# Kernel optimization log

Measured on AMD Instinct MI355X. Metric: run time of the kernel, lower is better.

## Reference

```python
import jax, jax.numpy as jnp
import numpy as np

D, H, L, N, BINS, V = 256, 8, 4, 512, 64, 20
DFF = 4 * D
DH = D // H
LAMBDA_RG = 10.0
STEPS = 10


def _lin(x, W, b):
    # torch nn.Linear convention: W is [out, in]
    return jnp.einsum('...i,oi->...o', x, W) + b


def _ln(x, g, b, eps=1e-5):
    m = x.mean(-1, keepdims=True)
    v = ((x - m) ** 2).mean(-1, keepdims=True)
    return (x - m) / jnp.sqrt(v + eps) * g + b


def _gelu(x):
    return jax.nn.gelu(x, approximate=False)  # torch nn.GELU default = exact erf


def _pos_encoding():
    pos = jnp.arange(N, dtype=jnp.float32)[:, None]
    div = jnp.exp(jnp.arange(0, D, 2, dtype=jnp.float32) * (-np.log(10000.0) / D))
    pe = jnp.zeros((N, D), jnp.float32)
    pe = pe.at[:, 0::2].set(jnp.sin(pos * div))
    pe = pe.at[:, 1::2].set(jnp.cos(pos * div))
    return pe


def _encoder_layer(x, Wqkv, bqkv, Wo, bo, g1, b1n, W1, b1, W2, b2, g2, b2n):
    # post-norm TransformerEncoderLayer, relu FFN, dropout=0 (eval)
    B, n, _ = x.shape
    qkv = _lin(x, Wqkv, bqkv)
    q, k, v = jnp.split(qkv, 3, axis=-1)
    hd = lambda t: t.reshape(B, n, H, DH).transpose(0, 2, 1, 3)
    q, k, v = hd(q), hd(k), hd(v)
    scores = jnp.einsum('bhqd,bhkd->bhqk', q, k) / jnp.sqrt(jnp.float32(DH))
    attn = jax.nn.softmax(scores, axis=-1)
    o = jnp.einsum('bhqk,bhkd->bhqd', attn, v).transpose(0, 2, 1, 3).reshape(B, n, D)
    x = _ln(x + _lin(o, Wo, bo), g1, b1n)
    ff = _lin(jax.nn.relu(_lin(x, W1, b1)), W2, b2)
    return _ln(x + ff, g2, b2n)


def setup_inputs() -> dict:
    key = jax.random.key(0)
    ks = list(jax.random.split(key, 24))
    it = iter(ks)
    w = lambda shape: jax.random.normal(next(it), shape, jnp.float32) * 0.02
    inp = {
        'tokens': jax.random.randint(next(it), (1, N), 0, V, dtype=jnp.int32),
        'noise': jax.random.normal(next(it), (1, N, 3), jnp.float32),
        'emb': w((V, D)),
        'Wqkv': w((L, 3 * D, D)), 'bqkv': jnp.zeros((L, 3 * D), jnp.float32),
        'Wo': w((L, D, D)), 'bo': jnp.zeros((L, D), jnp.float32),
        'ln1_g': jnp.ones((L, D), jnp.float32), 'ln1_b': jnp.zeros((L, D), jnp.float32),
        'W1': w((L, DFF, D)), 'b1': jnp.zeros((L, DFF), jnp.float32),
        'W2': w((L, D, DFF)), 'b2': jnp.zeros((L, D), jnp.float32),
        'ln2_g': jnp.ones((L, D), jnp.float32), 'ln2_b': jnp.zeros((L, D), jnp.float32),
        'aW1': w((D, D)), 'ab1': jnp.zeros((D,), jnp.float32),
        'aW2': w((1, D)), 'ab2': jnp.zeros((1,), jnp.float32),
        'cW': w((D, D)), 'cb': jnp.zeros((D,), jnp.float32),
        'dW1': w((D, 2 * D)), 'db1': jnp.zeros((D,), jnp.float32),
        'dW2': w((BINS, D)), 'db2': jnp.zeros((BINS,), jnp.float32),
        'tW1': w((D, D)), 'tb1': jnp.zeros((D,), jnp.float32),
        'tW2': w((2, D)), 'tb2': jnp.zeros((2,), jnp.float32),
        'pW': w((3, D)), 'pb': jnp.zeros((3,), jnp.float32),
    }
    return inp


def _forward(tokens, noise, emb, Wqkv, bqkv, Wo, bo, ln1_g, ln1_b, W1, b1, W2, b2,
             ln2_g, ln2_b, aW1, ab1, aW2, ab2, cW, cb, dW1, db1, dW2, db2,
             tW1, tb1, tW2, tb2, pW, pb):
    x = emb[tokens] + _pos_encoding()[None]  # [1,N,D]
    for l in range(L):
        x = _encoder_layer(x, Wqkv[l], bqkv[l], Wo[l], bo[l], ln1_g[l], ln1_b[l],
                           W1[l], b1[l], W2[l], b2[l], ln2_g[l], ln2_b[l])
    # AdaptiveAlphaPredictor
    a = jax.nn.sigmoid(_lin(_gelu(_lin(x, aW1, ab1)), aW2, ab2))
    alpha = (1.2 + a * (3.5 - 1.2))[..., 0]  # [1,N]
    # CSOCKernelAttention: distance power-law * exp-decay kernel
    idx = jnp.arange(N, dtype=jnp.float32)
    r = jnp.abs(idx[:, None] - idx[None, :]) + 1e-4  # [N,N]
    alpha_pair = (alpha[..., :, None] + alpha[..., None, :]) * 0.5  # [1,N,N]
    kernel = r[None] ** (-alpha_pair) * jnp.exp(-r[None] / LAMBDA_RG)
    kernel = kernel / (kernel.sum(-1, keepdims=True) + 1e-8)
    latent = jnp.einsum('bij,bjd->bid', kernel, x)
    # ContactPriorHead
    h = _lin(latent, cW, cb)
    contact = jax.nn.sigmoid(jnp.einsum('bid,bjd->bij', h, h))
    # DistogramHead: expand+concat+MLP (memory-bound O(N^2 d))
    xi = jnp.broadcast_to(latent[:, :, None, :], (1, N, N, D))
    xj = jnp.broadcast_to(latent[:, None, :, :], (1, N, N, D))
    pair = jnp.concatenate([xi, xj], axis=-1)  # [1,N,N,2D]
    disto = _lin(_gelu(_lin(pair, dW1, db1)), dW2, db2)  # [1,N,N,BINS]
    # TorsionGenerator
    t = _lin(_gelu(_lin(latent, tW1, tb1)), tW2, tb2)
    phi = jnp.tanh(t[..., 0]) * np.pi
    psi = jnp.tanh(t[..., 1]) * np.pi
    # DiffusionCoordinateInitializer (STEPS is a small fixed constant)
    target = _lin(latent, pW, pb)  # [1,N,3]
    c = noise
    for step in reversed(range(STEPS)):
        a_t = (step + 1) / STEPS
        c = a_t * c + (1.0 - a_t) * target
    return latent, alpha, contact, disto, phi, psi, c


def reference(tokens, noise, emb, Wqkv, bqkv, Wo, bo, ln1_g, ln1_b, W1, b1, W2, b2,
              ln2_g, ln2_b, aW1, ab1, aW2, ab2, cW, cb, dW1, db1, dW2, db2,
              tW1, tb1, tW2, tb2, pW, pb):
    return _forward(tokens, noise, emb, Wqkv, bqkv, Wo, bo, ln1_g, ln1_b, W1, b1,
                    W2, b2, ln2_g, ln2_b, aW1, ab1, aW2, ab2, cW, cb, dW1, db1,
                    dW2, db2, tW1, tb1, tW2, tb2, pW, pb)
```

## Files before the change

### kernel.cpp

```cpp
#include <hip/hip_runtime.h>
#include <hip/hip_bf16.h>

typedef __attribute__((ext_vector_type(8))) short bf16x8;
typedef __attribute__((ext_vector_type(4))) float f32x4;
typedef unsigned short ushort;

#define OFF_QKV 0
#define OFF_WO  786432
#define OFF_W1  1048576
#define OFF_W2  2097152
#define OFF_AW1 3145728
#define OFF_CW  3211264
#define OFF_DW1 3276800
#define OFF_TW1 3407872
#define WB_TOTAL 3473408

__device__ inline float gelu_f(float x) {
    return 0.5f * x * (1.0f + erff(x * 0.70710678118654752f));
}

__device__ inline ushort f2bfu(float x) {
    __hip_bfloat16 b = __float2bfloat16(x);
    return *reinterpret_cast<ushort*>(&b);
}

__device__ inline uint4 pack_bf8(float4 a, float4 b) {
    uint4 p;
    p.x = f2bfu(a.x) | ((unsigned)f2bfu(a.y) << 16);
    p.y = f2bfu(a.z) | ((unsigned)f2bfu(a.w) << 16);
    p.z = f2bfu(b.x) | ((unsigned)f2bfu(b.y) << 16);
    p.w = f2bfu(b.z) | ((unsigned)f2bfu(b.w) << 16);
    return p;
}

__device__ inline float wave_sum(float v) {
#pragma unroll
    for (int o = 32; o > 0; o >>= 1) v += __shfl_xor(v, o);
    return v;
}
__device__ inline float wave_max(float v) {
#pragma unroll
    for (int o = 32; o > 0; o >>= 1) v = fmaxf(v, __shfl_xor(v, o));
    return v;
}

__global__ void convw_k(const float* __restrict__ Wqkv, const float* __restrict__ Wo,
                        const float* __restrict__ W1, const float* __restrict__ W2,
                        const float* __restrict__ aW1, const float* __restrict__ cW,
                        const float* __restrict__ dW1, const float* __restrict__ tW1,
                        ushort* __restrict__ dst) {
    size_t i = ((size_t)blockIdx.x * 256 + threadIdx.x) * 8;
    if (i >= WB_TOTAL) return;
    const float* src;
    size_t off;
    if (i < OFF_WO)        { src = Wqkv; off = i; }
    else if (i < OFF_W1)   { src = Wo;   off = i - OFF_WO; }
    else if (i < OFF_W2)   { src = W1;   off = i - OFF_W1; }
    else if (i < OFF_AW1)  { src = W2;   off = i - OFF_W2; }
    else if (i < OFF_CW)   { src = aW1;  off = i - OFF_AW1; }
    else if (i < OFF_DW1)  { src = cW;   off = i - OFF_CW; }
    else if (i < OFF_TW1)  { src = dW1;  off = i - OFF_DW1; }
    else                   { src = tW1;  off = i - OFF_TW1; }
    float4 f0 = *(const float4*)&src[off];
    float4 f1 = *(const float4*)&src[off + 4];
    *(uint4*)&dst[i] = pack_bf8(f0, f1);
}

__global__ void embed_k(const int* __restrict__ tokens, const float* __restrict__ emb,
                        float* __restrict__ x, ushort* __restrict__ xb) {
    int n = blockIdx.x, t = threadIdx.x;
    float e = emb[(size_t)tokens[n] * 256 + t];
    int k = t >> 1;
    float div = expf((float)(2 * k) * (-9.210340371976184f / 256.0f));
    float arg = (float)n * div;
    float v = e + ((t & 1) ? cosf(arg) : sinf(arg));
    x[(size_t)n * 256 + t] = v;
    xb[(size_t)n * 256 + t] = f2bfu(v);
}

template <int ACT, int OBF>
__global__ __launch_bounds__(256) void gemm_bf(const ushort* __restrict__ A,
                                               const ushort* __restrict__ Wb,
                                               const float* __restrict__ bias,
                                               float* __restrict__ C,
                                               ushort* __restrict__ Cb,
                                               int Nn, int K, int lda, int ldw, int koff,
                                               size_t woff, size_t boff) {
    __shared__ ushort Al[2][2048];
    __shared__ ushort Wl[2][2048];
    const int t = threadIdx.x;
    const int bm = blockIdx.y * 64, bn = blockIdx.x * 64;
    const int lane = t & 63, wv = t >> 6;
    const int lo = lane & 15, hi = lane >> 4;

    const ushort* aptr = A + (size_t)(bm + lane) * lda + wv * 8;
    const ushort* wptr = Wb + woff + (size_t)(bn + lane) * ldw + koff + wv * 8;

    f32x4 acc0 = {0.f, 0.f, 0.f, 0.f}, acc1 = acc0, acc2 = acc0, acc3 = acc0;
    uint4 a = *(const uint4*)aptr;
    uint4 w = *(const uint4*)wptr;
    const int nsteps = K >> 5;
    for (int s = 0; s < nsteps; ++s) {
        const int buf = s & 1;
        *(uint4*)&Al[buf][t * 8] = a;
        *(uint4*)&Wl[buf][t * 8] = w;
        __syncthreads();
        if (s + 1 < nsteps) {
            a = *(const uint4*)(aptr + (s + 1) * 32);
            w = *(const uint4*)(wptr + (s + 1) * 32);
        }
        bf16x8 af = *(bf16x8*)&Al[buf][(hi * 64 + wv * 16 + lo) * 8];
        bf16x8 b0 = *(bf16x8*)&Wl[buf][(hi * 64 + 0 + lo) * 8];
        bf16x8 b1 = *(bf16x8*)&Wl[buf][(hi * 64 + 16 + lo) * 8];
        bf16x8 b2 = *(bf16x8*)&Wl[buf][(hi * 64 + 32 + lo) * 8];
        bf16x8 b3 = *(bf16x8*)&Wl[buf][(hi * 64 + 48 + lo) * 8];
        acc0 = __builtin_amdgcn_mfma_f32_16x16x32_bf16(af, b0, acc0, 0, 0, 0);
        acc1 = __builtin_amdgcn_mfma_f32_16x16x32_bf16(af, b1, acc1, 0, 0, 0);
        acc2 = __builtin_amdgcn_mfma_f32_16x16x32_bf16(af, b2, acc2, 0, 0, 0);
        acc3 = __builtin_amdgcn_mfma_f32_16x16x32_bf16(af, b3, acc3, 0, 0, 0);
    }

    float bv0 = bias ? bias[boff + bn + 0 + lo] : 0.0f;
    float bv1 = bias ? bias[boff + bn + 16 + lo] : 0.0f;
    float bv2 = bias ? bias[boff + bn + 32 + lo] : 0.0f;
    float bv3 = bias ? bias[boff + bn + 48 + lo] : 0.0f;
#pragma unroll
    for (int r = 0; r < 4; ++r) {
        size_t rw = (size_t)(bm + wv * 16 + hi * 4 + r) * Nn + bn;
        float v0 = acc0[r] + bv0, v1 = acc1[r] + bv1, v2 = acc2[r] + bv2, v3 = acc3[r] + bv3;
        if (ACT == 1) {
            v0 = fmaxf(v0, 0.f); v1 = fmaxf(v1, 0.f); v2 = fmaxf(v2, 0.f); v3 = fmaxf(v3, 0.f);
        }
        if (ACT == 2) {
            v0 = gelu_f(v0); v1 = gelu_f(v1); v2 = gelu_f(v2); v3 = gelu_f(v3);
        }
        if (OBF) {
            Cb[rw + 0 + lo] = f2bfu(v0);
            Cb[rw + 16 + lo] = f2bfu(v1);
            Cb[rw + 32 + lo] = f2bfu(v2);
            Cb[rw + 48 + lo] = f2bfu(v3);
        } else {
            C[rw + 0 + lo] = v0;
            C[rw + 16 + lo] = v1;
            C[rw + 32 + lo] = v2;
            C[rw + 48 + lo] = v3;
        }
    }
}

__global__ __launch_bounds__(256) void attn_k(const float* __restrict__ qkv,
                                              ushort* __restrict__ ob) {
    __shared__ float sc[4][512];
    int t = threadIdx.x;
    int w = t >> 6, lane = t & 63;
    int q = blockIdx.x * 4 + w;
    int h = blockIdx.y;
    const float* qptr = qkv + (size_t)q * 768 + h * 32;
    const float* kbase = qkv + 256 + h * 32;
    const float* vbase = qkv + 512 + h * 32;
    float qv[32];
#pragma unroll
    for (int d = 0; d < 32; d += 4) {
        float4 f = *(const float4*)(qptr + d);
        qv[d] = f.x; qv[d + 1] = f.y; qv[d + 2] = f.z; qv[d + 3] = f.w;
    }
    float mx = -1e30f;
    for (int k = lane; k < 512; k += 64) {
        const float* kp = kbase + (size_t)k * 768;
        float s = 0.0f;
#pragma unroll
        for (int d = 0; d < 32; d += 4) {
            float4 f = *(const float4*)(kp + d);
            s = fmaf(qv[d], f.x, s); s = fmaf(qv[d + 1], f.y, s);
            s = fmaf(qv[d + 2], f.z, s); s = fmaf(qv[d + 3], f.w, s);
        }
        s *= 0.17677669529663687f;
        sc[w][k] = s;
        mx = fmaxf(mx, s);
    }
    mx = wave_max(mx);
    float sum = 0.0f;
    for (int k = lane; k < 512; k += 64) {
        float e = expf(sc[w][k] - mx);
        sc[w][k] = e;
        sum += e;
    }
    sum = wave_sum(sum);
    float inv = 1.0f / sum;
    __syncthreads();
    int d = lane & 31, half = lane >> 5;
    const float* vp = vbase + d;
    const int kb = half * 256;
    float a0 = 0.f, a1 = 0.f, a2 = 0.f, a3 = 0.f;
    float a4 = 0.f, a5 = 0.f, a6 = 0.f, a7 = 0.f;
    for (int k = kb; k < kb + 256; k += 8) {
        float4 p0 = *(const float4*)&sc[w][k];
        float4 p1 = *(const float4*)&sc[w][k + 4];
        a0 = fmaf(p0.x, vp[(size_t)(k + 0) * 768], a0);
        a1 = fmaf(p0.y, vp[(size_t)(k + 1) * 768], a1);
        a2 = fmaf(p0.z, vp[(size_t)(k + 2) * 768], a2);
        a3 = fmaf(p0.w, vp[(size_t)(k + 3) * 768], a3);
        a4 = fmaf(p1.x, vp[(size_t)(k + 4) * 768], a4);
        a5 = fmaf(p1.y, vp[(size_t)(k + 5) * 768], a5);
        a6 = fmaf(p1.z, vp[(size_t)(k + 6) * 768], a6);
        a7 = fmaf(p1.w, vp[(size_t)(k + 7) * 768], a7);
    }
    float accv = ((a0 + a1) + (a2 + a3)) + ((a4 + a5) + (a6 + a7));
    accv += __shfl_down(accv, 32);
    if (lane < 32) ob[(size_t)q * 256 + h * 32 + d] = f2bfu(accv * inv);
}

__global__ void ln_res_k(float* __restrict__ x, const float* __restrict__ y,
                         const float* __restrict__ g, const float* __restrict__ b,
                         size_t goff, ushort* __restrict__ xb) {
    int row = blockIdx.x, t = threadIdx.x;
    __shared__ float red[8];
    float v = x[row * 256 + t] + y[row * 256 + t];
    float s = wave_sum(v);
    if ((t & 63) == 0) red[t >> 6] = s;
    __syncthreads();
    float mean = (red[0] + red[1] + red[2] + red[3]) * (1.0f / 256.0f);
    float d = v - mean;
    float s2 = wave_sum(d * d);
    if ((t & 63) == 0) red[4 + (t >> 6)] = s2;
    __syncthreads();
    float var = (red[4] + red[5] + red[6] + red[7]) * (1.0f / 256.0f);
    float res = d * rsqrtf(var + 1e-5f) * g[goff + t] + b[goff + t];
    x[row * 256 + t] = res;
    xb[row * 256 + t] = f2bfu(res);
}

__global__ void alpha_k(const float* __restrict__ t1, const float* __restrict__ aW2,
                        const float* __restrict__ ab2, float* __restrict__ alphaf,
                        float* __restrict__ out_alpha) {
    int t = threadIdx.x, w = t >> 6, lane = t & 63;
    int n = blockIdx.x * 4 + w;
    const float* r = t1 + (size_t)n * 256;
    float s = 0.0f;
    for (int d = lane; d < 256; d += 64) s = fmaf(r[d], aW2[d], s);
    s = wave_sum(s);
    if (lane == 0) {
        float z = s + ab2[0];
        float a = 1.0f / (1.0f + expf(-z));
        float al = 1.2f + 2.3f * a;
        alphaf[n] = al;
        out_alpha[n] = al;
    }
}

__global__ void csock_k(const float* __restrict__ x, const float* __restrict__ alphaf,
                        float* __restrict__ latent, float* __restrict__ out_latent,
                        ushort* __restrict__ latentb) {
    int i = blockIdx.x, t = threadIdx.x;
    __shared__ float wgt[512];
    __shared__ float red[4];
    float ai = alphaf[i];
    float lsum = 0.0f;
    for (int j = t; j < 512; j += 256) {
        float r = fabsf((float)(i - j)) + 1e-4f;
        float ap = 0.5f * (ai + alphaf[j]);
        float wv = powf(r, -ap) * expf(-r * 0.1f);
        wgt[j] = wv;
        lsum += wv;
    }
    float s = wave_sum(lsum);
    if ((t & 63) == 0) red[t >> 6] = s;
    __syncthreads();
    float S = red[0] + red[1] + red[2] + red[3] + 1e-8f;
    float acc = 0.0f;
    for (int j = 0; j < 512; ++j) acc = fmaf(wgt[j], x[(size_t)j * 256 + t], acc);
    float res = acc / S;
    latent[(size_t)i * 256 + t] = res;
    out_latent[(size_t)i * 256 + t] = res;
    latentb[(size_t)i * 256 + t] = f2bfu(res);
}

__global__ void contact_k(const float* __restrict__ h, float* __restrict__ out) {
    int i = blockIdx.x, t = threadIdx.x;
    __shared__ float hi[256];
    hi[t] = h[(size_t)i * 256 + t];
    __syncthreads();
    for (int j = t; j < 512; j += 256) {
        const float* hj = h + (size_t)j * 256;
        float s = 0.0f;
#pragma unroll 4
        for (int d = 0; d < 256; d += 4) {
            float4 a = *(const float4*)&hi[d];
            float4 b = *(const float4*)&hj[d];
            s = fmaf(a.x, b.x, s); s = fmaf(a.y, b.y, s);
            s = fmaf(a.z, b.z, s); s = fmaf(a.w, b.w, s);
        }
        out[(size_t)i * 512 + j] = 1.0f / (1.0f + expf(-s));
    }
}

__global__ __launch_bounds__(256) void disto_k(const float* __restrict__ U,
                                               const float* __restrict__ V,
                                               const float* __restrict__ dW2,
                                               const float* __restrict__ db2,
                                               float* __restrict__ out) {
    __shared__ short hsl[32 * 64 * 8];
    __shared__ short w2l[32 * 64 * 8];
    const int t = threadIdx.x;
    const int i = blockIdx.x;
    const int row = t >> 2;
    const int dq = t & 3;

#pragma unroll
    for (int c = 0; c < 8; ++c) {
        int dblk = dq * 8 + c;
        int d0 = dblk * 8;
        float4 w0 = *(const float4*)&dW2[(size_t)row * 256 + d0];
        float4 w1 = *(const float4*)&dW2[(size_t)row * 256 + d0 + 4];
        *(uint4*)&w2l[(dblk * 64 + row) * 8] = pack_bf8(w0, w1);
    }

    const int wv = t >> 6, lane = t & 63;
    const int lo = lane & 15, hi = lane >> 4;
    const int jw = wv * 16;
    float dbv[4];
#pragma unroll
    for (int nt = 0; nt < 4; ++nt) dbv[nt] = db2[nt * 16 + lo];

    for (int p = 0; p < 8; ++p) {
        const int j0 = p * 64;
#pragma unroll
        for (int c = 0; c < 8; ++c) {
            int dblk = dq * 8 + c;
            int d0 = dblk * 8;
            float4 u0 = *(const float4*)&U[(size_t)i * 256 + d0];
            float4 u1 = *(const float4*)&U[(size_t)i * 256 + d0 + 4];
            float4 v0 = *(const float4*)&V[(size_t)(j0 + row) * 256 + d0];
            float4 v1 = *(const float4*)&V[(size_t)(j0 + row) * 256 + d0 + 4];
            float4 h0, h1;
            h0.x = gelu_f(u0.x + v0.x); h0.y = gelu_f(u0.y + v0.y);
            h0.z = gelu_f(u0.z + v0.z); h0.w = gelu_f(u0.w + v0.w);
            h1.x = gelu_f(u1.x + v1.x); h1.y = gelu_f(u1.y + v1.y);
            h1.z = gelu_f(u1.z + v1.z); h1.w = gelu_f(u1.w + v1.w);
            *(uint4*)&hsl[(dblk * 64 + row) * 8] = pack_bf8(h0, h1);
        }
        __syncthreads();

        f32x4 acc0 = {0.f, 0.f, 0.f, 0.f}, acc1 = acc0, acc2 = acc0, acc3 = acc0;
#pragma unroll
        for (int kk = 0; kk < 8; ++kk) {
            int db = kk * 4 + hi;
            bf16x8 a = *(bf16x8*)&hsl[(db * 64 + jw + lo) * 8];
            bf16x8 b0 = *(bf16x8*)&w2l[(db * 64 + 0 + lo) * 8];
            bf16x8 b1 = *(bf16x8*)&w2l[(db * 64 + 16 + lo) * 8];
            bf16x8 b2 = *(bf16x8*)&w2l[(db * 64 + 32 + lo) * 8];
            bf16x8 b3 = *(bf16x8*)&w2l[(db * 64 + 48 + lo) * 8];
            acc0 = __builtin_amdgcn_mfma_f32_16x16x32_bf16(a, b0, acc0, 0, 0, 0);
            acc1 = __builtin_amdgcn_mfma_f32_16x16x32_bf16(a, b1, acc1, 0, 0, 0);
            acc2 = __builtin_amdgcn_mfma_f32_16x16x32_bf16(a, b2, acc2, 0, 0, 0);
            acc3 = __builtin_amdgcn_mfma_f32_16x16x32_bf16(a, b3, acc3, 0, 0, 0);
        }
#pragma unroll
        for (int r = 0; r < 4; ++r) {
            size_t jg = (size_t)i * 512 + j0 + jw + hi * 4 + r;
            out[jg * 64 + 0 + lo] = acc0[r] + dbv[0];
            out[jg * 64 + 16 + lo] = acc1[r] + dbv[1];
            out[jg * 64 + 32 + lo] = acc2[r] + dbv[2];
            out[jg * 64 + 48 + lo] = acc3[r] + dbv[3];
        }
        __syncthreads();
    }
}

__global__ void torsion_k(const float* __restrict__ t1, const float* __restrict__ tW2,
                          const float* __restrict__ tb2, float* __restrict__ phi,
                          float* __restrict__ psi) {
    int t = threadIdx.x, w = t >> 6, lane = t & 63;
    int n = blockIdx.x * 4 + w;
    const float* r = t1 + (size_t)n * 256;
    float s0 = 0.0f, s1 = 0.0f;
    for (int d = lane; d < 256; d += 64) {
        float v = r[d];
        s0 = fmaf(v, tW2[d], s0);
        s1 = fmaf(v, tW2[256 + d], s1);
    }
    s0 = wave_sum(s0);
    s1 = wave_sum(s1);
    if (lane == 0) {
        phi[n] = tanhf(s0 + tb2[0]) * 3.14159265358979323846f;
        psi[n] = tanhf(s1 + tb2[1]) * 3.14159265358979323846f;
    }
}

__global__ void diff_k(const float* __restrict__ latent, const float* __restrict__ pW,
                       const float* __restrict__ pb, const float* __restrict__ noise,
                       float* __restrict__ outc) {
    int idx = blockIdx.x * 256 + threadIdx.x;
    if (idx >= 512 * 3) return;
    int n = idx / 3, a = idx % 3;
    const float* r = latent + (size_t)n * 256;
    float s = pb[a];
    for (int d = 0; d < 256; ++d) s = fmaf(r[d], pW[(size_t)a * 256 + d], s);
    float c = noise[idx];
#pragma unroll
    for (int st = 9; st >= 0; --st) {
        float at = (float)(st + 1) * 0.1f;
        c = at * c + (1.0f - at) * s;
    }
    outc[idx] = c;
}

extern "C" void kernel_launch(void* const* d_in, const int* in_sizes, int n_in,
                              void* d_out, int out_size, void* d_ws, size_t ws_size,
                              hipStream_t stream) {
    const int* tokens  = (const int*)d_in[0];
    const float* noise = (const float*)d_in[1];
    const float* emb   = (const float*)d_in[2];
    const float* Wqkv  = (const float*)d_in[3];
    const float* bqkv  = (const float*)d_in[4];
    const float* Wo    = (const float*)d_in[5];
    const float* bo    = (const float*)d_in[6];
    const float* ln1_g = (const float*)d_in[7];
    const float* ln1_b = (const float*)d_in[8];
    const float* W1    = (const float*)d_in[9];
    const float* b1    = (const float*)d_in[10];
    const float* W2    = (const float*)d_in[11];
    const float* b2    = (const float*)d_in[12];
    const float* ln2_g = (const float*)d_in[13];
    const float* ln2_b = (const float*)d_in[14];
    const float* aW1   = (const float*)d_in[15];
    const float* ab1   = (const float*)d_in[16];
    const float* aW2   = (const float*)d_in[17];
    const float* ab2   = (const float*)d_in[18];
    const float* cW    = (const float*)d_in[19];
    const float* cb    = (const float*)d_in[20];
    const float* dW1   = (const float*)d_in[21];
    const float* db1   = (const float*)d_in[22];
    const float* dW2   = (const float*)d_in[23];
    const float* db2   = (const float*)d_in[24];
    const float* tW1   = (const float*)d_in[25];
    const float* tb1   = (const float*)d_in[26];
    const float* tW2   = (const float*)d_in[27];
    const float* tb2   = (const float*)d_in[28];
    const float* pW    = (const float*)d_in[29];
    const float* pb    = (const float*)d_in[30];

    float* out         = (float*)d_out;
    float* out_latent  = out;
    float* out_alpha   = out + 131072;
    float* out_contact = out + 131584;
    float* out_disto   = out + 393728;
    float* out_phi     = out + 17170944;
    float* out_psi     = out + 17171456;
    float* out_c       = out + 17171968;

    float* scratch = out_disto;
    float* x    = scratch;
    float* qkv  = scratch + 131072;
    float* y    = scratch + 1179648;
    float* hbuf = scratch + 1310720;
    float* t1   = scratch + 1441792;
    ushort* wb      = (ushort*)(scratch + 2000000);
    ushort* xb      = (ushort*)(scratch + 3740000);
    ushort* ob      = (ushort*)(scratch + 3810000);
    ushort* ffhb    = (ushort*)(scratch + 3880000);
    ushort* latentb = (ushort*)(scratch + 4150000);

    float* latentf = (float*)d_ws;
    float* U       = latentf + 131072;
    float* Vv      = U + 131072;
    float* alphaf  = Vv + 131072;

    convw_k<<<1696, 256, 0, stream>>>(Wqkv, Wo, W1, W2, aW1, cW, dW1, tW1, wb);
    embed_k<<<512, 256, 0, stream>>>(tokens, emb, x, xb);

    for (int l = 0; l < 4; ++l) {
        gemm_bf<0, 0><<<dim3(12, 8), 256, 0, stream>>>(xb, wb, bqkv, qkv, nullptr,
                                                       768, 256, 256, 256, 0,
                                                       OFF_QKV + (size_t)l * 196608, (size_t)l * 768);
        attn_k<<<dim3(128, 8), 256, 0, stream>>>(qkv, ob);
        gemm_bf<0, 0><<<dim3(4, 8), 256, 0, stream>>>(ob, wb, bo, y, nullptr,
                                                      256, 256, 256, 256, 0,
                                                      OFF_WO + (size_t)l * 65536, (size_t)l * 256);
        ln_res_k<<<512, 256, 0, stream>>>(x, y, ln1_g, ln1_b, (size_t)l * 256, xb);
        gemm_bf<1, 1><<<dim3(16, 8), 256, 0, stream>>>(xb, wb, b1, nullptr, ffhb,
                                                       1024, 256, 256, 256, 0,
                                                       OFF_W1 + (size_t)l * 262144, (size_t)l * 1024);
        gemm_bf<0, 0><<<dim3(4, 8), 256, 0, stream>>>(ffhb, wb, b2, y, nullptr,
                                                      256, 1024, 1024, 1024, 0,
                                                      OFF_W2 + (size_t)l * 262144, (size_t)l * 256);
        ln_res_k<<<512, 256, 0, stream>>>(x, y, ln2_g, ln2_b, (size_t)l * 256, xb);
    }

    gemm_bf<2, 0><<<dim3(4, 8), 256, 0, stream>>>(xb, wb, ab1, t1, nullptr,
                                                  256, 256, 256, 256, 0, OFF_AW1, 0);
    alpha_k<<<128, 256, 0, stream>>>(t1, aW2, ab2, alphaf, out_alpha);

    csock_k<<<512, 256, 0, stream>>>(x, alphaf, latentf, out_latent, latentb);

    gemm_bf<0, 0><<<dim3(4, 8), 256, 0, stream>>>(latentb, wb, cb, hbuf, nullptr,
                                                  256, 256, 256, 256, 0, OFF_CW, 0);
    contact_k<<<512, 256, 0, stream>>>(hbuf, out_contact);

    gemm_bf<0, 0><<<dim3(4, 8), 256, 0, stream>>>(latentb, wb, db1, U, nullptr,
                                                  256, 256, 256, 512, 0, OFF_DW1, 0);
    gemm_bf<0, 0><<<dim3(4, 8), 256, 0, stream>>>(latentb, wb, nullptr, Vv, nullptr,
                                                  256, 256, 256, 512, 256, OFF_DW1, 0);

    gemm_bf<2, 0><<<dim3(4, 8), 256, 0, stream>>>(latentb, wb, tb1, t1, nullptr,
                                                  256, 256, 256, 256, 0, OFF_TW1, 0);
    torsion_k<<<128, 256, 0, stream>>>(t1, tW2, tb2, out_phi, out_psi);

    diff_k<<<6, 256, 0, stream>>>(latentf, pW, pb, noise, out_c);

    disto_k<<<512, 256, 0, stream>>>(U, Vv, dW2, db2, out_disto);
}
```

Measured before the change: 509.1 us.

## Fuse O-projection and FFN with residual LayerNorm; batch head GEMMs into one launch

```diff
diff --git a/kernel.cpp b/kernel.cpp
--- a/kernel.cpp
+++ b/kernel.cpp
@@ -148,6 +148,283 @@
     }
 }
 
+__global__ __launch_bounds__(256) void oproj_ln_k(const ushort* __restrict__ ob,
+                                                  const ushort* __restrict__ wbp,
+                                                  const float* __restrict__ bo,
+                                                  const float* __restrict__ g,
+                                                  const float* __restrict__ bln,
+                                                  float* __restrict__ x,
+                                                  ushort* __restrict__ xb,
+                                                  size_t woff, size_t boff, size_t goff) {
+    __shared__ ushort Al[2][2048];
+    __shared__ ushort Wl[2][8192];
+    const int t = threadIdx.x;
+    const int bm = blockIdx.x * 64;
+    const int lane = t & 63, wv = t >> 6;
+    const int lo = lane & 15, hi = lane >> 4;
+    const int arow = t >> 2, akg = t & 3;
+
+    const ushort* aptr = ob + (size_t)(bm + arow) * 256 + akg * 8;
+    const ushort* wptr = wbp + woff + akg * 8;
+
+    f32x4 acc[16];
+#pragma unroll
+    for (int i = 0; i < 16; ++i) acc[i] = (f32x4){0.f, 0.f, 0.f, 0.f};
+
+    uint4 apre = *(const uint4*)aptr;
+    uint4 wpre[4];
+#pragma unroll
+    for (int q = 0; q < 4; ++q)
+        wpre[q] = *(const uint4*)(wptr + (size_t)(q * 64 + arow) * 256);
+
+    for (int s = 0; s < 8; ++s) {
+        const int buf = s & 1;
+        *(uint4*)&Al[buf][(akg * 64 + arow) * 8] = apre;
+#pragma unroll
+        for (int q = 0; q < 4; ++q)
+            *(uint4*)&Wl[buf][(akg * 256 + q * 64 + arow) * 8] = wpre[q];
+        __syncthreads();
+        if (s < 7) {
+            apre = *(const uint4*)(aptr + (s + 1) * 32);
+#pragma unroll
+            for (int q = 0; q < 4; ++q)
+                wpre[q] = *(const uint4*)(wptr + (size_t)(q * 64 + arow) * 256 + (s + 1) * 32);
+        }
+        bf16x8 af = *(bf16x8*)&Al[buf][(hi * 64 + wv * 16 + lo) * 8];
+#pragma unroll
+        for (int nt = 0; nt < 16; ++nt) {
+            bf16x8 bf = *(bf16x8*)&Wl[buf][(hi * 256 + nt * 16 + lo) * 8];
+            acc[nt] = __builtin_amdgcn_mfma_f32_16x16x32_bf16(af, bf, acc[nt], 0, 0, 0);
+        }
+    }
+
+    float bv[16], gg[16], bb[16];
+#pragma unroll
+    for (int nt = 0; nt < 16; ++nt) {
+        bv[nt] = bo[boff + nt * 16 + lo];
+        gg[nt] = g[goff + nt * 16 + lo];
+        bb[nt] = bln[goff + nt * 16 + lo];
+    }
+#pragma unroll
+    for (int r = 0; r < 4; ++r) {
+        int row = bm + wv * 16 + hi * 4 + r;
+        float part = 0.f;
+#pragma unroll
+        for (int nt = 0; nt < 16; ++nt) {
+            float xo = x[(size_t)row * 256 + nt * 16 + lo];
+            float v = acc[nt][r] + bv[nt] + xo;
+            acc[nt][r] = v;
+            part += v;
+        }
+        part += __shfl_xor(part, 1); part += __shfl_xor(part, 2);
+        part += __shfl_xor(part, 4); part += __shfl_xor(part, 8);
+        float mean = part * (1.0f / 256.0f);
+        float p2 = 0.f;
+#pragma unroll
+        for (int nt = 0; nt < 16; ++nt) { float d = acc[nt][r] - mean; p2 = fmaf(d, d, p2); }
+        p2 += __shfl_xor(p2, 1); p2 += __shfl_xor(p2, 2);
+        p2 += __shfl_xor(p2, 4); p2 += __shfl_xor(p2, 8);
+        float inv = rsqrtf(p2 * (1.0f / 256.0f) + 1e-5f);
+#pragma unroll
+        for (int nt = 0; nt < 16; ++nt) {
+            float res = (acc[nt][r] - mean) * inv * gg[nt] + bb[nt];
+            x[(size_t)row * 256 + nt * 16 + lo] = res;
+            xb[(size_t)row * 256 + nt * 16 + lo] = f2bfu(res);
+        }
+    }
+}
+
+__global__ __launch_bounds__(256) void ffn_ln_k(const ushort* __restrict__ xbin,
+                                                const ushort* __restrict__ wbp,
+                                                const float* __restrict__ b1,
+                                                const float* __restrict__ b2,
+                                                const float* __restrict__ g,
+                                                const float* __restrict__ bln,
+                                                float* __restrict__ x,
+                                                ushort* __restrict__ xb,
+                                                size_t w1off, size_t w2off,
+                                                size_t b1off, size_t b2off, size_t goff) {
+    __shared__ ushort Hl[32768];
+    __shared__ ushort Al[2][2048];
+    __shared__ ushort W1l[2][2048];
+    __shared__ ushort W2l[2][8192];
+    const int t = threadIdx.x;
+    const int bm = blockIdx.x * 64;
+    const int lane = t & 63, wv = t >> 6;
+    const int lo = lane & 15, hi = lane >> 4;
+    const int arow = t >> 2, akg = t & 3;
+    const ushort* aptr = xbin + (size_t)(bm + arow) * 256 + akg * 8;
+
+    f32x4 yacc[16];
+#pragma unroll
+    for (int i = 0; i < 16; ++i) yacc[i] = (f32x4){0.f, 0.f, 0.f, 0.f};
+
+    for (int half = 0; half < 2; ++half) {
+        for (int p = 0; p < 8; ++p) {
+            const int colbase = half * 512 + p * 64;
+            const ushort* w1ptr = wbp + w1off + (size_t)(colbase + arow) * 256 + akg * 8;
+            f32x4 pacc[4];
+#pragma unroll
+            for (int i = 0; i < 4; ++i) pacc[i] = (f32x4){0.f, 0.f, 0.f, 0.f};
+            uint4 apre = *(const uint4*)aptr;
+            uint4 w1pre = *(const uint4*)w1ptr;
+            for (int s = 0; s < 8; ++s) {
+                const int buf = s & 1;
+                *(uint4*)&Al[buf][(akg * 64 + arow) * 8] = apre;
+                *(uint4*)&W1l[buf][(akg * 64 + arow) * 8] = w1pre;
+                __syncthreads();
+                if (s < 7) {
+                    apre = *(const uint4*)(aptr + (s + 1) * 32);
+                    w1pre = *(const uint4*)(w1ptr + (s + 1) * 32);
+                }
+                bf16x8 af = *(bf16x8*)&Al[buf][(hi * 64 + wv * 16 + lo) * 8];
+#pragma unroll
+                for (int nt = 0; nt < 4; ++nt) {
+                    bf16x8 bf = *(bf16x8*)&W1l[buf][(hi * 64 + nt * 16 + lo) * 8];
+                    pacc[nt] = __builtin_amdgcn_mfma_f32_16x16x32_bf16(af, bf, pacc[nt], 0, 0, 0);
+                }
+            }
+#pragma unroll
+            for (int nt = 0; nt < 4; ++nt) {
+                float bvv = b1[b1off + colbase + nt * 16 + lo];
+#pragma unroll
+                for (int r = 0; r < 4; ++r) {
+                    float v = fmaxf(pacc[nt][r] + bvv, 0.f);
+                    int row = wv * 16 + hi * 4 + r;
+                    int cl = p * 64 + nt * 16 + lo;
+                    Hl[((cl >> 3) * 64 + row) * 8 + (cl & 7)] = f2bfu(v);
+                }
+            }
+        }
+        __syncthreads();
+
+        const ushort* w2ptr = wbp + w2off + (size_t)half * 512 + akg * 8;
+        uint4 w2pre[4];
+#pragma unroll
+        for (int q = 0; q < 4; ++q)
+            w2pre[q] = *(const uint4*)(w2ptr + (size_t)(q * 64 + arow) * 1024);
+        for (int s = 0; s < 16; ++s) {
+            const int buf = s & 1;
+#pragma unroll
+            for (int q = 0; q < 4; ++q)
+                *(uint4*)&W2l[buf][(akg * 256 + q * 64 + arow) * 8] = w2pre[q];
+            __syncthreads();
+            if (s < 15) {
+#pragma unroll
+                for (int q = 0; q < 4; ++q)
+                    w2pre[q] = *(const uint4*)(w2ptr + (size_t)(q * 64 + arow) * 1024 + (s + 1) * 32);
+            }
+            bf16x8 af = *(bf16x8*)&Hl[((s * 4 + hi) * 64 + wv * 16 + lo) * 8];
+#pragma unroll
+            for (int nt = 0; nt < 16; ++nt) {
+                bf16x8 bf = *(bf16x8*)&W2l[buf][(hi * 256 + nt * 16 + lo) * 8];
+                yacc[nt] = __builtin_amdgcn_mfma_f32_16x16x32_bf16(af, bf, yacc[nt], 0, 0, 0);
+            }
+        }
+        __syncthreads();
+    }
+
+    float bv[16], gg[16], bb[16];
+#pragma unroll
+    for (int nt = 0; nt < 16; ++nt) {
+        bv[nt] = b2[b2off + nt * 16 + lo];
+        gg[nt] = g[goff + nt * 16 + lo];
+        bb[nt] = bln[goff + nt * 16 + lo];
+    }
+#pragma unroll
+    for (int r = 0; r < 4; ++r) {
+        int row = bm + wv * 16 + hi * 4 + r;
+        float part = 0.f;
+#pragma unroll
+        for (int nt = 0; nt < 16; ++nt) {
+            float xo = x[(size_t)row * 256 + nt * 16 + lo];
+            float v = yacc[nt][r] + bv[nt] + xo;
+            yacc[nt][r] = v;
+            part += v;
+        }
+        part += __shfl_xor(part, 1); part += __shfl_xor(part, 2);
+        part += __shfl_xor(part, 4); part += __shfl_xor(part, 8);
+        float mean = part * (1.0f / 256.0f);
+        float p2 = 0.f;
+#pragma unroll
+        for (int nt = 0; nt < 16; ++nt) { float d = yacc[nt][r] - mean; p2 = fmaf(d, d, p2); }
+        p2 += __shfl_xor(p2, 1); p2 += __shfl_xor(p2, 2);
+        p2 += __shfl_xor(p2, 4); p2 += __shfl_xor(p2, 8);
+        float inv = rsqrtf(p2 * (1.0f / 256.0f) + 1e-5f);
+#pragma unroll
+        for (int nt = 0; nt < 16; ++nt) {
+            float res = (yacc[nt][r] - mean) * inv * gg[nt] + bb[nt];
+            x[(size_t)row * 256 + nt * 16 + lo] = res;
+            xb[(size_t)row * 256 + nt * 16 + lo] = f2bfu(res);
+        }
+    }
+}
+
+__global__ __launch_bounds__(256) void heads_k(const ushort* __restrict__ A,
+                                               const ushort* __restrict__ Wb,
+                                               const float* __restrict__ cb,
+                                               const float* __restrict__ db1,
+                                               const float* __restrict__ tb1,
+                                               float* __restrict__ hbuf,
+                                               float* __restrict__ U,
+                                               float* __restrict__ Vv,
+                                               float* __restrict__ t1t) {
+    size_t woff; int ldw, koff, act; const float* bias; float* C;
+    const int z = blockIdx.z;
+    if (z == 0)      { woff = OFF_CW;  ldw = 256; koff = 0;   bias = cb;      act = 0; C = hbuf; }
+    else if (z == 1) { woff = OFF_DW1; ldw = 512; koff = 0;   bias = db1;     act = 0; C = U; }
+    else if (z == 2) { woff = OFF_DW1; ldw = 512; koff = 256; bias = nullptr; act = 0; C = Vv; }
+    else             { woff = OFF_TW1; ldw = 256; koff = 0;   bias = tb1;     act = 2; C = t1t; }
+
+    __shared__ ushort Al[2][2048];
+    __shared__ ushort Wl[2][2048];
+    const int t = threadIdx.x;
+    const int bm = blockIdx.y * 64, bn = blockIdx.x * 64;
+    const int lane = t & 63, wv = t >> 6;
+    const int lo = lane & 15, hi = lane >> 4;
+
+    const ushort* aptr = A + (size_t)(bm + lane) * 256 + wv * 8;
+    const ushort* wptr = Wb + woff + (size_t)(bn + lane) * ldw + koff + wv * 8;
+
+    f32x4 acc0 = {0.f, 0.f, 0.f, 0.f}, acc1 = acc0, acc2 = acc0, acc3 = acc0;
+    uint4 a = *(const uint4*)aptr;
+    uint4 w = *(const uint4*)wptr;
+    for (int s = 0; s < 8; ++s) {
+        const int buf = s & 1;
+        *(uint4*)&Al[buf][t * 8] = a;
+        *(uint4*)&Wl[buf][t * 8] = w;
+        __syncthreads();
+        if (s < 7) {
+            a = *(const uint4*)(aptr + (s + 1) * 32);
+            w = *(const uint4*)(wptr + (s + 1) * 32);
+        }
+        bf16x8 af = *(bf16x8*)&Al[buf][(hi * 64 + wv * 16 + lo) * 8];
+        bf16x8 b0 = *(bf16x8*)&Wl[buf][(hi * 64 + 0 + lo) * 8];
+        bf16x8 b1 = *(bf16x8*)&Wl[buf][(hi * 64 + 16 + lo) * 8];
+        bf16x8 b2 = *(bf16x8*)&Wl[buf][(hi * 64 + 32 + lo) * 8];
+        bf16x8 b3 = *(bf16x8*)&Wl[buf][(hi * 64 + 48 + lo) * 8];
+        acc0 = __builtin_amdgcn_mfma_f32_16x16x32_bf16(af, b0, acc0, 0, 0, 0);
+        acc1 = __builtin_amdgcn_mfma_f32_16x16x32_bf16(af, b1, acc1, 0, 0, 0);
+        acc2 = __builtin_amdgcn_mfma_f32_16x16x32_bf16(af, b2, acc2, 0, 0, 0);
+        acc3 = __builtin_amdgcn_mfma_f32_16x16x32_bf16(af, b3, acc3, 0, 0, 0);
+    }
+
+    float bv0 = bias ? bias[bn + 0 + lo] : 0.0f;
+    float bv1 = bias ? bias[bn + 16 + lo] : 0.0f;
+    float bv2 = bias ? bias[bn + 32 + lo] : 0.0f;
+    float bv3 = bias ? bias[bn + 48 + lo] : 0.0f;
+#pragma unroll
+    for (int r = 0; r < 4; ++r) {
+        size_t rw = (size_t)(bm + wv * 16 + hi * 4 + r) * 256 + bn;
+        float v0 = acc0[r] + bv0, v1 = acc1[r] + bv1, v2 = acc2[r] + bv2, v3 = acc3[r] + bv3;
+        if (act == 2) { v0 = gelu_f(v0); v1 = gelu_f(v1); v2 = gelu_f(v2); v3 = gelu_f(v3); }
+        C[rw + 0 + lo] = v0;
+        C[rw + 16 + lo] = v1;
+        C[rw + 32 + lo] = v2;
+        C[rw + 48 + lo] = v3;
+    }
+}
+
 __global__ __launch_bounds__(256) void attn_k(const float* __restrict__ qkv,
                                               ushort* __restrict__ ob) {
     __shared__ float sc[4][512];
@@ -208,26 +485,6 @@
     float accv = ((a0 + a1) + (a2 + a3)) + ((a4 + a5) + (a6 + a7));
     accv += __shfl_down(accv, 32);
     if (lane < 32) ob[(size_t)q * 256 + h * 32 + d] = f2bfu(accv * inv);
-}
-
-__global__ void ln_res_k(float* __restrict__ x, const float* __restrict__ y,
-                         const float* __restrict__ g, const float* __restrict__ b,
-                         size_t goff, ushort* __restrict__ xb) {
-    int row = blockIdx.x, t = threadIdx.x;
-    __shared__ float red[8];
-    float v = x[row * 256 + t] + y[row * 256 + t];
-    float s = wave_sum(v);
-    if ((t & 63) == 0) red[t >> 6] = s;
-    __syncthreads();
-    float mean = (red[0] + red[1] + red[2] + red[3]) * (1.0f / 256.0f);
-    float d = v - mean;
-    float s2 = wave_sum(d * d);
-    if ((t & 63) == 0) red[4 + (t >> 6)] = s2;
-    __syncthreads();
-    float var = (red[4] + red[5] + red[6] + red[7]) * (1.0f / 256.0f);
-    float res = d * rsqrtf(var + 1e-5f) * g[goff + t] + b[goff + t];
-    x[row * 256 + t] = res;
-    xb[row * 256 + t] = f2bfu(res);
 }
 
 __global__ void alpha_k(const float* __restrict__ t1, const float* __restrict__ aW2,
@@ -452,13 +709,12 @@
     float* scratch = out_disto;
     float* x    = scratch;
     float* qkv  = scratch + 131072;
-    float* y    = scratch + 1179648;
+    float* t1t  = scratch + 655360;
     float* hbuf = scratch + 1310720;
-    float* t1   = scratch + 1441792;
+    float* t1a  = scratch + 1441792;
     ushort* wb      = (ushort*)(scratch + 2000000);
     ushort* xb      = (ushort*)(scratch + 3740000);
     ushort* ob      = (ushort*)(scratch + 3810000);
-    ushort* ffhb    = (ushort*)(scratch + 3880000);
     ushort* latentb = (ushort*)(scratch + 4150000);
 
     float* latentf = (float*)d_ws;
@@ -474,37 +730,27 @@
                                                        768, 256, 256, 256, 0,
                                                        OFF_QKV + (size_t)l * 196608, (size_t)l * 768);
         attn_k<<<dim3(128, 8), 256, 0, stream>>>(qkv, ob);
-        gemm_bf<0, 0><<<dim3(4, 8), 256, 0, stream>>>(ob, wb, bo, y, nullptr,
-                                                      256, 256, 256, 256, 0,
-                                                      OFF_WO + (size_t)l * 65536, (size_t)l * 256);
-        ln_res_k<<<512, 256, 0, stream>>>(x, y, ln1_g, ln1_b, (size_t)l * 256, xb);
-        gemm_bf<1, 1><<<dim3(16, 8), 256, 0, stream>>>(xb, wb, b1, nullptr, ffhb,
-                                                       1024, 256, 256, 256, 0,
-                                                       OFF_W1 + (size_t)l * 262144, (size_t)l * 1024);
-        gemm_bf<0, 0><<<dim3(4, 8), 256, 0, stream>>>(ffhb, wb, b2, y, nullptr,
-                                                      256, 1024, 1024, 1024, 0,
-                                                      OFF_W2 + (size_t)l * 262144, (size_t)l * 256);
-        ln_res_k<<<512, 256, 0, stream>>>(x, y, ln2_g, ln2_b, (size_t)l * 256, xb);
-    }
-
-    gemm_bf<2, 0><<<dim3(4, 8), 256, 0, stream>>>(xb, wb, ab1, t1, nullptr,
+        oproj_ln_k<<<8, 256, 0, stream>>>(ob, wb, bo, ln1_g, ln1_b, x, xb,
+                                          OFF_WO + (size_t)l * 65536, (size_t)l * 256,
+                                          (size_t)l * 256);
+        ffn_ln_k<<<8, 256, 0, stream>>>(xb, wb, b1, b2, ln2_g, ln2_b, x, xb,
+                                        OFF_W1 + (size_t)l * 262144,
+                                        OFF_W2 + (size_t)l * 262144,
+                                        (size_t)l * 1024, (size_t)l * 256,
+                                        (size_t)l * 256);
+    }
+
+    gemm_bf<2, 0><<<dim3(4, 8), 256, 0, stream>>>(xb, wb, ab1, t1a, nullptr,
                                                   256, 256, 256, 256, 0, OFF_AW1, 0);
-    alpha_k<<<128, 256, 0, stream>>>(t1, aW2, ab2, alphaf, out_alpha);
+    alpha_k<<<128, 256, 0, stream>>>(t1a, aW2, ab2, alphaf, out_alpha);
 
     csock_k<<<512, 256, 0, stream>>>(x, alphaf, latentf, out_latent, latentb);
 
-    gemm_bf<0, 0><<<dim3(4, 8), 256, 0, stream>>>(latentb, wb, cb, hbuf, nullptr,
-                                                  256, 256, 256, 256, 0, OFF_CW, 0);
+    heads_k<<<dim3(4, 8, 4), 256, 0, stream>>>(latentb, wb, cb, db1, tb1,
+                                               hbuf, U, Vv, t1t);
+
     contact_k<<<512, 256, 0, stream>>>(hbuf, out_contact);
-
-    gemm_bf<0, 0><<<dim3(4, 8), 256, 0, stream>>>(latentb, wb, db1, U, nullptr,
-                                                  256, 256, 256, 512, 0, OFF_DW1, 0);
-    gemm_bf<0, 0><<<dim3(4, 8), 256, 0, stream>>>(latentb, wb, nullptr, Vv, nullptr,
-                                                  256, 256, 256, 512, 256, OFF_DW1, 0);
-
-    gemm_bf<2, 0><<<dim3(4, 8), 256, 0, stream>>>(latentb, wb, tb1, t1, nullptr,
-                                                  256, 256, 256, 256, 0, OFF_TW1, 0);
-    torsion_k<<<128, 256, 0, stream>>>(t1, tW2, tb2, out_phi, out_psi);
+    torsion_k<<<128, 256, 0, stream>>>(t1t, tW2, tb2, out_phi, out_psi);
 
     diff_k<<<6, 256, 0, stream>>>(latentf, pW, pb, noise, out_c);
 
```

New measurement: 752.6 us. 47.8% more time.
